# Performance work log

Measured on AMD Instinct MI355X. Metric: run time of the kernel, lower is better.

Reference implementation:

```python
import jax, jax.numpy as jnp
import numpy as np

H, HKV, D, HID = 64, 8, 64, 2880
T = 2048
WINDOW = 128
THETA = 150000.0
FACTOR = 32.0
ORIG_MAX = 4096
BETA_FAST, BETA_SLOW = 32.0, 1.0
EPS = 1e-5
SCALE = D ** -0.5
MSCALE = float(0.1 * np.log(FACTOR) + 1.0)  # vLLM YaRN attention mscale


def _yarn_inv_freq():
    # vLLM YaRNScalingRotaryEmbedding inverse frequencies
    def corr_dim(n_rot):
        return D * np.log(ORIG_MAX / (n_rot * 2.0 * np.pi)) / (2.0 * np.log(THETA))
    low = max(int(np.floor(corr_dim(BETA_FAST))), 0)
    high = min(int(np.ceil(corr_dim(BETA_SLOW))), D - 1)
    pow_ = np.arange(0, D, 2, dtype=np.float32) / D
    extrap = 1.0 / (THETA ** pow_)                 # extrapolation inv_freq
    interp = extrap / FACTOR                        # interpolation inv_freq
    ramp = np.clip((np.arange(D // 2, dtype=np.float32) - low) / max(high - low, 1e-3), 0.0, 1.0)
    extrap_mask = 1.0 - ramp
    inv_freq = interp * (1.0 - extrap_mask) + extrap * extrap_mask
    return jnp.asarray(inv_freq, jnp.float32)

_INV_FREQ = _yarn_inv_freq()


def _rope(positions, x):
    # neox-style rotation; x: [T, heads, D]
    freqs = positions.astype(jnp.float32)[:, None] * _INV_FREQ[None, :]  # [T, D/2]
    cos = (jnp.cos(freqs) * MSCALE)[:, None, :]
    sin = (jnp.sin(freqs) * MSCALE)[:, None, :]
    x1, x2 = x[..., : D // 2], x[..., D // 2 :]
    return jnp.concatenate([x1 * cos - x2 * sin, x2 * cos + x1 * sin], axis=-1)


def _attn(q, k, v, sinks):
    # q: [T,H,D]; k,v: [T,HKV,D]; sinks: [H] extra softmax logit per head
    g = H // HKV
    k = jnp.repeat(k, g, axis=1)
    v = jnp.repeat(v, g, axis=1)
    scores = jnp.einsum('qhd,khd->hqk', q, k) * SCALE  # [H,T,T]
    i = jnp.arange(T)[:, None]
    j = jnp.arange(T)[None, :]
    mask = (j <= i) & (i - j < WINDOW)  # causal + sliding window (even layer)
    scores = jnp.where(mask[None], scores, -jnp.inf)
    s = sinks[:, None]                                    # [H,1]
    m = jnp.maximum(jnp.max(scores, axis=-1), s)          # [H,T]
    p = jnp.exp(scores - m[..., None])                    # [H,T,T]
    denom = jnp.sum(p, axis=-1) + jnp.exp(s - m)          # sink adds to denominator only
    out = jnp.einsum('hqk,khd->qhd', p, v) / denom.T[..., None]
    return out.reshape(T, H * D)


def setup_inputs() -> dict:
    key = jax.random.key(0)
    ks = jax.random.split(key, 8)
    return {
        'hidden_states': jax.random.normal(ks[0], (T, HID), jnp.float32),
        'positions': jnp.arange(T, dtype=jnp.int32),
        'norm_w': jnp.ones((HID,), jnp.float32),
        'w_qkv': jax.random.normal(ks[1], ((H + 2 * HKV) * D, HID), jnp.float32) * 0.02,
        'b_qkv': jax.random.normal(ks[2], ((H + 2 * HKV) * D,), jnp.float32) * 0.02,
        'w_o': jax.random.normal(ks[3], (HID, H * D), jnp.float32) * 0.02,
        'b_o': jax.random.normal(ks[4], (HID,), jnp.float32) * 0.02,
        'sinks': jax.random.normal(ks[5], (H,), jnp.float32),
    }


def reference(hidden_states, positions, norm_w, w_qkv, b_qkv, w_o, b_o, sinks):
    x = hidden_states
    t = x * jax.lax.rsqrt(jnp.mean(x * x, axis=-1, keepdims=True) + EPS) * norm_w  # RMSNorm
    qkv = t @ w_qkv.T + b_qkv
    q, k, v = jnp.split(qkv, [H * D, H * D + HKV * D], axis=-1)
    q = _rope(positions, q.reshape(T, H, D))
    k = _rope(positions, k.reshape(T, HKV, D))
    v = v.reshape(T, HKV, D)
    attn_out = _attn(q, k, v, sinks)
    out = attn_out @ w_o.T + b_o
    return out + x  # residual
```

## Files before the change

kernel.cpp:

```cpp
#include <hip/hip_runtime.h>
#include <hip/hip_bf16.h>
#include <stdint.h>

typedef __attribute__((ext_vector_type(8))) short bf16x8;
typedef __attribute__((ext_vector_type(8))) unsigned short u16x8;
typedef __attribute__((ext_vector_type(4))) float f32x4;
typedef __attribute__((ext_vector_type(4))) unsigned short u16x4;

#define T_SEQ 2048
#define HID_D 2880
#define KPAD 2944
#define NH 64
#define NKV 8
#define HD 64
#define QKV_N 5120
#define ATT_N 4096
#define NOPAD 3072
#define WIN 128
#define RSCALE 0.125f
#define MSCALE 1.3465735903f
#define ROPE_TOT (T_SEQ * (NH + NKV) * 32)

__device__ __forceinline__ unsigned short f2bf(float f) {
  union { float f; unsigned u; } v; v.f = f;
  unsigned r = v.u + 0x7fffu + ((v.u >> 16) & 1u);
  return (unsigned short)(r >> 16);
}
__device__ __forceinline__ float bf2f(unsigned short u) {
  union { unsigned u; float f; } v; v.u = ((unsigned)u) << 16;
  return v.f;
}

__device__ __forceinline__ void gload_lds16(const void* g, void* l) {
  __builtin_amdgcn_global_load_lds((const __attribute__((address_space(1))) char*)g,
                                   (__attribute__((address_space(3))) char*)l, 16, 0, 0);
}

__global__ __launch_bounds__(256) void pre_kernel(const float* __restrict__ x,
                                                  const float* __restrict__ w,
                                                  unsigned short* __restrict__ t_bf,
                                                  const float* __restrict__ wq_src,
                                                  unsigned short* __restrict__ wq_dst) {
  __shared__ float red[256];
  if (blockIdx.x < 2048) {
    int row = blockIdx.x;
    const float4* xr4 = (const float4*)(x + (size_t)row * HID_D);
    const float4* w4 = (const float4*)w;
    float ss = 0.f;
    for (int i = threadIdx.x; i < 720; i += 256) {
      float4 v = xr4[i];
      ss += v.x * v.x + v.y * v.y + v.z * v.z + v.w * v.w;
    }
    red[threadIdx.x] = ss;
    __syncthreads();
    for (int s = 128; s > 0; s >>= 1) {
      if (threadIdx.x < s) red[threadIdx.x] += red[threadIdx.x + s];
      __syncthreads();
    }
    float rs = rsqrtf(red[0] / (float)HID_D + 1e-5f);
    u16x4* ob = (u16x4*)(t_bf + (size_t)row * KPAD);
    for (int i = threadIdx.x; i < 736; i += 256) {
      u16x4 o = {0, 0, 0, 0};
      if (i < 720) {
        float4 v = xr4[i];
        float4 g = w4[i];
        o = { f2bf(v.x * rs * g.x), f2bf(v.y * rs * g.y),
              f2bf(v.z * rs * g.z), f2bf(v.w * rs * g.w) };
      }
      ob[i] = o;
    }
  } else {
    const int total = QKV_N * 736;
    for (int i = (blockIdx.x - 2048) * 256 + threadIdx.x; i < total; i += 1024 * 256) {
      int c4 = i % 736, row = i / 736;
      u16x4 o = {0, 0, 0, 0};
      if (c4 < 720) {
        float4 v = ((const float4*)wq_src)[(size_t)row * 720 + c4];
        o = { f2bf(v.x), f2bf(v.y), f2bf(v.z), f2bf(v.w) };
      }
      ((u16x4*)wq_dst)[i] = o;
    }
  }
}

__device__ __forceinline__ void gemm_body(const unsigned short* __restrict__ A,
                                          const unsigned short* __restrict__ B,
                                          unsigned short* __restrict__ C,
                                          const float* __restrict__ bias,
                                          int N, int ld, int nt,
                                          int nbx, int nstore, int swz,
                                          unsigned short* sA, unsigned short* sB) {
  const int tid = threadIdx.x;
  const int lane = tid & 63, wid = tid >> 6;
  const int wr = wid >> 2, wc = wid & 3;
  const int lq = lane & 15, ro = lane >> 4;

  const int bx = swz % nbx, by = swz / nbx;
  const int m0 = by * 256, n0 = bx * 256;

  const int R0 = tid >> 3;
  const int g0 = (((tid & 7) ^ (R0 & 7)) << 3);
  const size_t aOff = (size_t)(m0 + R0) * ld + g0;
  size_t bOff[2][2];
#pragma unroll
  for (int h = 0; h < 2; ++h)
#pragma unroll
    for (int r = 0; r < 2; ++r) {
      int rr = n0 + h * 128 + r * 64 + R0;
      bOff[h][r] = (size_t)rr * ld + g0;
    }

  const int ck0 = ((ro ^ (lq & 7)) << 3);
  const int ck1 = (((4 + ro) ^ (lq & 7)) << 3);

#define STG_A(BUF, H, KT)                                                        \
  { unsigned short* _d = sA + ((BUF) * 2 + (H)) * 8192 + wid * 512;              \
    const unsigned short* _s = A + aOff + (size_t)((H) * 128) * ld + (KT) * 64;  \
    gload_lds16(_s, _d); gload_lds16(_s + (size_t)64 * ld, _d + 4096); }
#define STG_B(BUF, H, KT)                                                        \
  { unsigned short* _d = sB + ((BUF) * 2 + (H)) * 8192 + wid * 512;              \
    gload_lds16(B + bOff[H][0] + (KT) * 64, _d);                                 \
    gload_lds16(B + bOff[H][1] + (KT) * 64, _d + 4096); }

  bf16x8 aR[8];
  bf16x8 bR0[4], bR1[4];
  f32x4 acc[8][4] = {};

#define LDA(BUF, S)                                                                        \
  { _Pragma("unroll") for (int ii = 0; ii < 4; ++ii) {                                     \
      const int _r = ((BUF) * 2 + wr) * 8192 + ((S) * 64 + ii * 16 + lq) * 64;             \
      aR[ii * 2 + 0] = *(const bf16x8*)&sA[_r + ck0];                                      \
      aR[ii * 2 + 1] = *(const bf16x8*)&sA[_r + ck1]; } }
#define LDB(BUF, NHF, DST)                                                                 \
  { _Pragma("unroll") for (int jj = 0; jj < 2; ++jj) {                                     \
      const int _r = ((BUF) * 2 + (wc >> 1)) * 8192 +                                      \
                     ((wc & 1) * 64 + ((NHF) * 2 + jj) * 16 + lq) * 64;                    \
      DST[jj * 2 + 0] = *(const bf16x8*)&sB[_r + ck0];                                     \
      DST[jj * 2 + 1] = *(const bf16x8*)&sB[_r + ck1]; } }
#define MFMA16(S, NHF, BREG)                                                               \
  { _Pragma("unroll") for (int ii = 0; ii < 4; ++ii)                                       \
    _Pragma("unroll") for (int jj = 0; jj < 2; ++jj)                                       \
    _Pragma("unroll") for (int kk = 0; kk < 2; ++kk)                                       \
      acc[(S) * 4 + ii][(NHF) * 2 + jj] = __builtin_amdgcn_mfma_f32_16x16x32_bf16(         \
          aR[ii * 2 + kk], BREG[jj * 2 + kk], acc[(S) * 4 + ii][(NHF) * 2 + jj], 0, 0, 0); }
#define PH_MID()                                         \
  __builtin_amdgcn_s_barrier();                          \
  asm volatile("s_waitcnt lgkmcnt(0)" ::: "memory");     \
  __builtin_amdgcn_sched_barrier(0);                     \
  __builtin_amdgcn_s_setprio(1)
#define PH_END()                                         \
  __builtin_amdgcn_s_setprio(0);                         \
  __builtin_amdgcn_s_barrier()

  STG_A(0, 0, 0); STG_A(0, 1, 0); STG_B(0, 0, 0); STG_B(0, 1, 0);
  STG_B(1, 0, 1); STG_B(1, 1, 1);
  asm volatile("s_waitcnt vmcnt(4)" ::: "memory");
  __builtin_amdgcn_s_barrier();

  const int niter = nt >> 1;
  for (int it = 0; it < niter; ++it) {
    const int t = it * 2;
    const bool more = (it + 1 < niter);
    LDA(0, 0); LDB(0, 0, bR0); STG_A(1, 0, t + 1);
    PH_MID(); MFMA16(0, 0, bR0); PH_END();
    LDB(0, 1, bR1); STG_A(1, 1, t + 1);
    PH_MID(); MFMA16(0, 1, bR1); PH_END();
    LDA(0, 1); if (more) STG_B(0, 0, t + 2);
    PH_MID(); MFMA16(1, 1, bR1); PH_END();
    if (more) STG_B(0, 1, t + 2);
    PH_MID(); MFMA16(1, 0, bR0);
    __builtin_amdgcn_s_setprio(0);
    if (more) asm volatile("s_waitcnt vmcnt(4)" ::: "memory");
    else      asm volatile("s_waitcnt vmcnt(0)" ::: "memory");
    __builtin_amdgcn_s_barrier();
    LDA(1, 0); LDB(1, 0, bR0); if (more) STG_A(0, 0, t + 2);
    PH_MID(); MFMA16(0, 0, bR0); PH_END();
    LDB(1, 1, bR1); if (more) STG_A(0, 1, t + 2);
    PH_MID(); MFMA16(0, 1, bR1); PH_END();
    LDA(1, 1); if (more) STG_B(1, 0, t + 3);
    PH_MID(); MFMA16(1, 1, bR1); PH_END();
    if (more) STG_B(1, 1, t + 3);
    PH_MID(); MFMA16(1, 0, bR0);
    __builtin_amdgcn_s_setprio(0);
    if (more) asm volatile("s_waitcnt vmcnt(4)" ::: "memory");
    else      asm volatile("s_waitcnt vmcnt(0)" ::: "memory");
    __builtin_amdgcn_s_barrier();
  }
#undef STG_A
#undef STG_B
#undef LDA
#undef LDB
#undef MFMA16

#pragma unroll
  for (int fi = 0; fi < 8; ++fi) {
    const int gr = m0 + wr * 128 + fi * 16 + ro * 4;
#pragma unroll
    for (int j = 0; j < 4; ++j) {
      const int gc = n0 + wc * 64 + j * 16 + lq;
      const float bv = bias[gc];
#pragma unroll
      for (int r = 0; r < 4; ++r)
        C[(size_t)(gr + r) * nstore + gc] = f2bf(acc[fi][j][r] + bv);
    }
  }
}

__global__ __launch_bounds__(512, 2) void qkv_fused_kernel(const unsigned short* __restrict__ A,
                                                           const unsigned short* __restrict__ B,
                                                           unsigned short* __restrict__ C,
                                                           const float* __restrict__ bias,
                                                           const float* __restrict__ wo_src,
                                                           unsigned short* __restrict__ wo_dst) {
  __shared__ unsigned short sA[2 * 2 * 128 * 64];
  __shared__ unsigned short sB[2 * 2 * 128 * 64];
  const int c = blockIdx.x & 7, q = blockIdx.x >> 3;
  if (q < 20) {
    const int by = (c & 1) * 4 + (q & 3);
    const int bx = (c >> 1) * 5 + (q >> 2);
    gemm_body(A, B, C, bias, QKV_N, KPAD, 46, 20, QKV_N, by * 20 + bx, sA, sB);
  } else {
    const int cid = c * 12 + (q - 20);
    const int total = HID_D * 1024;
    for (int i = cid * 512 + threadIdx.x; i < total; i += 96 * 512) {
      float4 v = ((const float4*)wo_src)[i];
      u16x4 o = { f2bf(v.x), f2bf(v.y), f2bf(v.z), f2bf(v.w) };
      ((u16x4*)wo_dst)[i] = o;
    }
  }
}

__global__ __launch_bounds__(512, 2) void outproj192_kernel(const unsigned short* __restrict__ att,
                                                            const unsigned short* __restrict__ wo,
                                                            float* __restrict__ out,
                                                            const float* __restrict__ b_o,
                                                            const float* __restrict__ x) {
  __shared__ unsigned short sA[2 * 128 * 64];
  __shared__ unsigned short sB[3 * 192 * 64];

  const int tid = threadIdx.x;
  const int lane = tid & 63, wid = tid >> 6;
  const int wr = wid >> 2, wc = wid & 3;
  const int lq = lane & 15, ro = lane >> 4;

  const int c = blockIdx.x & 7, q = blockIdx.x >> 3;
  const int by = c * 2 + (q >= 15 ? 1 : 0);
  const int bx = (q >= 15) ? q - 15 : q;
  const int m0 = by * 128, n0 = bx * 192;

  const int R0 = tid >> 3;
  const int g0 = (((tid & 7) ^ (R0 & 7)) << 3);
  const size_t aOff = (size_t)(m0 + R0) * ATT_N + g0;
  size_t bOff[3];
#pragma unroll
  for (int r = 0; r < 3; ++r)
    bOff[r] = (size_t)(n0 + r * 64 + R0) * ATT_N + g0;

  const int ck0 = ((ro ^ (lq & 7)) << 3);
  const int ck1 = (((4 + ro) ^ (lq & 7)) << 3);

#define PSTG_A(BUF, KT)                                                         \
  { unsigned short* _d = sA + (BUF) * 8192 + wid * 512;                         \
    const unsigned short* _s = att + aOff + (size_t)(KT) * 64;                  \
    gload_lds16(_s, _d); gload_lds16(_s + (size_t)64 * ATT_N, _d + 4096); }
#define PSTG_B(BUF, KT)                                                         \
  { unsigned short* _d = sB + (BUF) * 12288 + wid * 512;                        \
    gload_lds16(wo + bOff[0] + (KT) * 64, _d);                                  \
    gload_lds16(wo + bOff[1] + (KT) * 64, _d + 4096);                           \
    gload_lds16(wo + bOff[2] + (KT) * 64, _d + 8192); }

  bf16x8 aR[8];
  bf16x8 b00, b01, b10, b11, b20, b21;
  f32x4 acc[4][3] = {};

#define PLDA(BUF)                                                                          \
  { _Pragma("unroll") for (int ii = 0; ii < 4; ++ii) {                                     \
      const int _r = (BUF) * 8192 + (wr * 64 + ii * 16 + lq) * 64;                         \
      aR[ii * 2 + 0] = *(const bf16x8*)&sA[_r + ck0];                                      \
      aR[ii * 2 + 1] = *(const bf16x8*)&sA[_r + ck1]; } }
#define PLDB(BUF, J, D0, D1)                                                               \
  { const int _r = (BUF) * 12288 + (wc * 48 + (J) * 16 + lq) * 64;                         \
    D0 = *(const bf16x8*)&sB[_r + ck0];                                                    \
    D1 = *(const bf16x8*)&sB[_r + ck1]; }

  PSTG_B(0, 0); PSTG_A(0, 0);
  PSTG_B(1, 1); PSTG_A(1, 1);
  asm volatile("s_waitcnt vmcnt(5)" ::: "memory");
  __builtin_amdgcn_s_barrier();

  const int nt = 64;
  for (int T = 0; T < nt; ++T) {
    const bool more = (T + 2 < nt);
    const int bb = T % 3, bA = T & 1;
    PLDA(bA);
    PLDB(bb, 0, b00, b01);
    PLDB(bb, 1, b10, b11);
    if (more) PSTG_B((T + 2) % 3, T + 2);
    PH_MID();
#pragma unroll
    for (int ii = 0; ii < 4; ++ii) {
      acc[ii][0] = __builtin_amdgcn_mfma_f32_16x16x32_bf16(aR[ii * 2 + 0], b00, acc[ii][0], 0, 0, 0);
      acc[ii][0] = __builtin_amdgcn_mfma_f32_16x16x32_bf16(aR[ii * 2 + 1], b01, acc[ii][0], 0, 0, 0);
      acc[ii][1] = __builtin_amdgcn_mfma_f32_16x16x32_bf16(aR[ii * 2 + 0], b10, acc[ii][1], 0, 0, 0);
      acc[ii][1] = __builtin_amdgcn_mfma_f32_16x16x32_bf16(aR[ii * 2 + 1], b11, acc[ii][1], 0, 0, 0);
    }
    PH_END();
    PLDB(bb, 2, b20, b21);
    if (more) PSTG_A((T + 2) & 1, T + 2);
    PH_MID();
#pragma unroll
    for (int ii = 0; ii < 4; ++ii) {
      acc[ii][2] = __builtin_amdgcn_mfma_f32_16x16x32_bf16(aR[ii * 2 + 0], b20, acc[ii][2], 0, 0, 0);
      acc[ii][2] = __builtin_amdgcn_mfma_f32_16x16x32_bf16(aR[ii * 2 + 1], b21, acc[ii][2], 0, 0, 0);
    }
    __builtin_amdgcn_s_setprio(0);
    if (more) asm volatile("s_waitcnt vmcnt(5)" ::: "memory");
    else      asm volatile("s_waitcnt vmcnt(0)" ::: "memory");
    __builtin_amdgcn_s_barrier();
  }
#undef PSTG_A
#undef PSTG_B
#undef PLDA
#undef PLDB
#undef PH_MID
#undef PH_END

#pragma unroll
  for (int ii = 0; ii < 4; ++ii) {
    const int gr = m0 + wr * 64 + ii * 16 + ro * 4;
#pragma unroll
    for (int j = 0; j < 3; ++j) {
      const int gc = n0 + wc * 48 + j * 16 + lq;
      const float bv = b_o[gc];
#pragma unroll
      for (int r = 0; r < 4; ++r) {
        size_t off = (size_t)(gr + r) * HID_D + gc;
        out[off] = acc[ii][j][r] + bv + x[off];
      }
    }
  }
}

__global__ __launch_bounds__(256) void ropev_kernel(const unsigned short* __restrict__ qkvb,
                                                    const int* __restrict__ positions,
                                                    unsigned short* __restrict__ qb,
                                                    unsigned short* __restrict__ kb) {
  int idx = blockIdx.x * 256 + threadIdx.x;
  int d = idx & 31;
  int head = (idx >> 5) % (NH + NKV);
  int t = idx / ((NH + NKV) * 32);
  float pw = (float)d * (1.0f / 32.0f);
  float extrap = expf(-pw * 11.9183905733f);
  float interp = extrap * (1.0f / 32.0f);
  float ramp = fminf(fmaxf(((float)d - 8.0f) * 0.1f, 0.0f), 1.0f);
  float invf = interp * ramp + extrap * (1.0f - ramp);
  float fr = (float)positions[t] * invf;
  float s, c;
  sincosf(fr, &s, &c);
  c *= MSCALE;
  s *= MSCALE;
  if (head < NH) {
    const unsigned short* b = qkvb + (size_t)t * QKV_N + head * HD + d;
    float x1 = bf2f(b[0]), x2 = bf2f(b[32]);
    unsigned short* ob = qb + (size_t)t * ATT_N + head * HD + d;
    ob[0] = f2bf(x1 * c - x2 * s);
    ob[32] = f2bf(x2 * c + x1 * s);
  } else {
    int gk = head - NH;
    const unsigned short* b = qkvb + (size_t)t * QKV_N + NH * HD + gk * HD + d;
    float x1 = bf2f(b[0]), x2 = bf2f(b[32]);
    unsigned short* ob = kb + (size_t)t * (NKV * HD) + gk * HD + d;
    ob[0] = f2bf(x1 * c - x2 * s);
    ob[32] = f2bf(x2 * c + x1 * s);
  }
}

__global__ __launch_bounds__(256) void vtrans_kernel(const unsigned short* __restrict__ qkvb,
                                                     unsigned short* __restrict__ vt) {
  __shared__ unsigned short tile[64][72];
  const int g = blockIdx.x >> 5;
  const int t0 = (blockIdx.x & 31) << 6;
  const int r = threadIdx.x >> 3;
  const int c8 = (threadIdx.x & 7) << 3;
  const size_t vbase = (size_t)(NH + NKV) * HD + (size_t)g * HD;
#pragma unroll
  for (int hh = 0; hh < 2; ++hh) {
    int row = r + hh * 32;
    *(u16x8*)&tile[row][c8] =
        *(const u16x8*)(qkvb + (size_t)(t0 + row) * QKV_N + vbase + c8);
  }
  __syncthreads();
  const int d = threadIdx.x >> 2;
  const int ts = (threadIdx.x & 3) << 4;
  u16x8 v0, v1;
#pragma unroll
  for (int i = 0; i < 8; ++i) { v0[i] = tile[ts + i][d]; v1[i] = tile[ts + 8 + i][d]; }
  unsigned short* dst = vt + (size_t)(g * HD + d) * T_SEQ + t0 + ts;
  *(u16x8*)dst = v0;
  *(u16x8*)(dst + 8) = v1;
}

__global__ __launch_bounds__(256) void attn_kernel(const unsigned short* __restrict__ qb,
                                                   const unsigned short* __restrict__ kb,
                                                   const unsigned short* __restrict__ vt,
                                                   const float* __restrict__ sinks,
                                                   unsigned short* __restrict__ att) {
  __shared__ unsigned short orep[4][16][72];
  const int lane = threadIdx.x & 63;
  const int wid = threadIdx.x >> 6;
  const int q0 = blockIdx.x * 16;
  const int h = blockIdx.y * 4 + wid;
  const int g = h >> 3;
  const int lq = lane & 15;
  const int ro = lane >> 4;

  bf16x8 bq0, bq1;
  {
    const unsigned short* qp = qb + (size_t)(q0 + lq) * ATT_N + h * HD + ro * 8;
    bq0 = *(const bf16x8*)qp;
    bq1 = *(const bf16x8*)(qp + 32);
  }
  float m_run = sinks[h];
  float l_run = 1.0f;
  f32x4 o0 = {0.f, 0.f, 0.f, 0.f}, o1 = o0, o2 = o0, o3 = o0;
  const int qg = q0 + lq;
  const int jstart = (q0 >= WIN) ? q0 - WIN : 0;

  for (int jt = jstart; jt <= q0; jt += 32) {
    f32x4 st0 = {0.f, 0.f, 0.f, 0.f}, st1 = st0;
    {
      int kr = jt + ((lq >> 2) << 3) + (lq & 3);
      int kr0 = min(kr, T_SEQ - 1);
      int kr1 = min(kr + 4, T_SEQ - 1);
      const unsigned short* kp0 = kb + (size_t)kr0 * (NKV * HD) + g * HD + ro * 8;
      const unsigned short* kp1 = kb + (size_t)kr1 * (NKV * HD) + g * HD + ro * 8;
      bf16x8 ka0a = *(const bf16x8*)kp0;
      bf16x8 ka0b = *(const bf16x8*)(kp0 + 32);
      bf16x8 ka1a = *(const bf16x8*)kp1;
      bf16x8 ka1b = *(const bf16x8*)(kp1 + 32);
      st0 = __builtin_amdgcn_mfma_f32_16x16x32_bf16(ka0a, bq0, st0, 0, 0, 0);
      st0 = __builtin_amdgcn_mfma_f32_16x16x32_bf16(ka0b, bq1, st0, 0, 0, 0);
      st1 = __builtin_amdgcn_mfma_f32_16x16x32_bf16(ka1a, bq0, st1, 0, 0, 0);
      st1 = __builtin_amdgcn_mfma_f32_16x16x32_bf16(ka1b, bq1, st1, 0, 0, 0);
    }
    float p[8];
    float tmax = -3.0e30f;
#pragma unroll
    for (int r = 0; r < 4; ++r) {
      int jg0 = jt + ro * 8 + r;
      int jg1 = jg0 + 4;
      float s0 = (jg0 <= qg && (qg - jg0) < WIN) ? st0[r] * RSCALE : -3.0e30f;
      float s1 = (jg1 <= qg && (qg - jg1) < WIN) ? st1[r] * RSCALE : -3.0e30f;
      p[r] = s0;
      p[r + 4] = s1;
      tmax = fmaxf(tmax, fmaxf(s0, s1));
    }
    tmax = fmaxf(tmax, __shfl_xor(tmax, 16));
    tmax = fmaxf(tmax, __shfl_xor(tmax, 32));
    float m_new = fmaxf(m_run, tmax);
    float rescale = expf(m_run - m_new);
    float psum = 0.f;
    bf16x8 pa;
#pragma unroll
    for (int jj = 0; jj < 8; ++jj) {
      float pe = expf(p[jj] - m_new);
      psum += pe;
      pa[jj] = (short)f2bf(pe);
    }
    psum += __shfl_xor(psum, 16);
    psum += __shfl_xor(psum, 32);
    l_run = l_run * rescale + psum;
    m_run = m_new;
    f32x4 rs4;
#pragma unroll
    for (int r = 0; r < 4; ++r) rs4[r] = __shfl(rescale, ro * 4 + r);
    o0 *= rs4; o1 *= rs4; o2 *= rs4; o3 *= rs4;
    int tb = jt + ro * 8;
    if (tb > T_SEQ - 8) tb = T_SEQ - 8;
    const unsigned short* vp = vt + (size_t)(g * HD + lq) * T_SEQ + tb;
    bf16x8 v0 = *(const bf16x8*)vp;
    bf16x8 v1 = *(const bf16x8*)(vp + 16 * T_SEQ);
    bf16x8 v2 = *(const bf16x8*)(vp + 32 * T_SEQ);
    bf16x8 v3 = *(const bf16x8*)(vp + 48 * T_SEQ);
    o0 = __builtin_amdgcn_mfma_f32_16x16x32_bf16(pa, v0, o0, 0, 0, 0);
    o1 = __builtin_amdgcn_mfma_f32_16x16x32_bf16(pa, v1, o1, 0, 0, 0);
    o2 = __builtin_amdgcn_mfma_f32_16x16x32_bf16(pa, v2, o2, 0, 0, 0);
    o3 = __builtin_amdgcn_mfma_f32_16x16x32_bf16(pa, v3, o3, 0, 0, 0);
  }

#pragma unroll
  for (int r = 0; r < 4; ++r) {
    float lr = __shfl(l_run, ro * 4 + r);
    float inv = 1.0f / lr;
    int row = ro * 4 + r;
    orep[wid][row][lq]      = f2bf(o0[r] * inv);
    orep[wid][row][lq + 16] = f2bf(o1[r] * inv);
    orep[wid][row][lq + 32] = f2bf(o2[r] * inv);
    orep[wid][row][lq + 48] = f2bf(o3[r] * inv);
  }
  {
    const int row = lane >> 2;
    const int seg = (lane & 3) << 4;
    u16x8 w0 = *(const u16x8*)&orep[wid][row][seg];
    u16x8 w1 = *(const u16x8*)&orep[wid][row][seg + 8];
    unsigned short* op = att + (size_t)(q0 + row) * ATT_N + h * HD + seg;
    *(u16x8*)op = w0;
    *(u16x8*)(op + 8) = w1;
  }
}

extern "C" void kernel_launch(void* const* d_in, const int* in_sizes, int n_in,
                              void* d_out, int out_size, void* d_ws, size_t ws_size,
                              hipStream_t stream) {
  const float* x = (const float*)d_in[0];
  const int* pos = (const int*)d_in[1];
  const float* norm_w = (const float*)d_in[2];
  const float* w_qkv = (const float*)d_in[3];
  const float* b_qkv = (const float*)d_in[4];
  const float* w_o = (const float*)d_in[5];
  const float* b_o = (const float*)d_in[6];
  const float* sinks = (const float*)d_in[7];
  float* out = (float*)d_out;

  unsigned short* t_bf = (unsigned short*)d_ws;
  unsigned short* wq_bf = t_bf + (size_t)T_SEQ * KPAD;
  unsigned short* wo_bf = wq_bf + (size_t)QKV_N * KPAD;
  unsigned short* qkv_bf = wo_bf + (size_t)NOPAD * ATT_N;
  unsigned short* qb = qkv_bf + (size_t)T_SEQ * QKV_N;
  unsigned short* kb = qb + (size_t)T_SEQ * ATT_N;
  unsigned short* vt = kb + (size_t)T_SEQ * NKV * HD;
  unsigned short* att = vt + (size_t)NKV * HD * T_SEQ;

  pre_kernel<<<3072, 256, 0, stream>>>(x, norm_w, t_bf, w_qkv, wq_bf);
  qkv_fused_kernel<<<256, 512, 0, stream>>>(t_bf, wq_bf, qkv_bf, b_qkv, w_o, wo_bf);
  ropev_kernel<<<ROPE_TOT / 256, 256, 0, stream>>>(qkv_bf, pos, qb, kb);
  vtrans_kernel<<<256, 256, 0, stream>>>(qkv_bf, vt);
  attn_kernel<<<dim3(T_SEQ / 16, NH / 4), 256, 0, stream>>>(qb, kb, vt, sinks, att);
  outproj192_kernel<<<240, 512, 0, stream>>>(att, wo_bf, out, b_o, x);
}
```

Before: 229.2 us.

## Retile QKV GEMM to 128x320 blocks and move w_o conversion into attention launch

The QKV projection GEMM moves from 160 blocks of 256x256 tiles to 256 blocks of 128x320 tiles with a triple-buffered B stage. This fills all 256 workgroup slots with GEMM work instead of reserving 96 blocks for the w_o fp32-to-bf16 conversion. That conversion is moved into 128 extra blocks prepended to the attention launch, which is flattened to a 1D grid. The intent is better CU balance for the GEMM, at the cost of lower per-block arithmetic intensity and extra work inside the attention kernel.

```diff
diff --git a/kernel.cpp b/kernel.cpp
--- a/kernel.cpp
+++ b/kernel.cpp
@@ -35,6 +35,15 @@
   __builtin_amdgcn_global_load_lds((const __attribute__((address_space(1))) char*)g,
                                    (__attribute__((address_space(3))) char*)l, 16, 0, 0);
 }
+
+#define GPH_MID()                                        \
+  __builtin_amdgcn_s_barrier();                          \
+  asm volatile("s_waitcnt lgkmcnt(0)" ::: "memory");     \
+  __builtin_amdgcn_sched_barrier(0);                     \
+  __builtin_amdgcn_s_setprio(1)
+#define GPH_END()                                        \
+  __builtin_amdgcn_s_setprio(0);                         \
+  __builtin_amdgcn_s_barrier()
 
 __global__ __launch_bounds__(256) void pre_kernel(const float* __restrict__ x,
                                                   const float* __restrict__ w,
@@ -83,149 +92,110 @@
   }
 }
 
-__device__ __forceinline__ void gemm_body(const unsigned short* __restrict__ A,
-                                          const unsigned short* __restrict__ B,
-                                          unsigned short* __restrict__ C,
-                                          const float* __restrict__ bias,
-                                          int N, int ld, int nt,
-                                          int nbx, int nstore, int swz,
-                                          unsigned short* sA, unsigned short* sB) {
+__global__ __launch_bounds__(512, 2) void qkv320_kernel(const unsigned short* __restrict__ A,
+                                                        const unsigned short* __restrict__ B,
+                                                        unsigned short* __restrict__ C,
+                                                        const float* __restrict__ bias) {
+  __shared__ unsigned short sA[2 * 128 * 64];
+  __shared__ unsigned short sB[3 * 320 * 64];
+
   const int tid = threadIdx.x;
   const int lane = tid & 63, wid = tid >> 6;
   const int wr = wid >> 2, wc = wid & 3;
   const int lq = lane & 15, ro = lane >> 4;
 
-  const int bx = swz % nbx, by = swz / nbx;
-  const int m0 = by * 256, n0 = bx * 256;
+  const int c = blockIdx.x & 7, q = blockIdx.x >> 3;
+  const int by = (c & 1) * 8 + (q & 7);
+  const int bx = (c >> 1) * 4 + (q >> 3);
+  const int m0 = by * 128, n0 = bx * 320;
 
   const int R0 = tid >> 3;
   const int g0 = (((tid & 7) ^ (R0 & 7)) << 3);
-  const size_t aOff = (size_t)(m0 + R0) * ld + g0;
-  size_t bOff[2][2];
-#pragma unroll
-  for (int h = 0; h < 2; ++h)
-#pragma unroll
-    for (int r = 0; r < 2; ++r) {
-      int rr = n0 + h * 128 + r * 64 + R0;
-      bOff[h][r] = (size_t)rr * ld + g0;
-    }
+  const size_t aOff = (size_t)(m0 + R0) * KPAD + g0;
+  size_t bOff[5];
+#pragma unroll
+  for (int r = 0; r < 5; ++r)
+    bOff[r] = (size_t)(n0 + r * 64 + R0) * KPAD + g0;
 
   const int ck0 = ((ro ^ (lq & 7)) << 3);
   const int ck1 = (((4 + ro) ^ (lq & 7)) << 3);
 
-#define STG_A(BUF, H, KT)                                                        \
-  { unsigned short* _d = sA + ((BUF) * 2 + (H)) * 8192 + wid * 512;              \
-    const unsigned short* _s = A + aOff + (size_t)((H) * 128) * ld + (KT) * 64;  \
-    gload_lds16(_s, _d); gload_lds16(_s + (size_t)64 * ld, _d + 4096); }
-#define STG_B(BUF, H, KT)                                                        \
-  { unsigned short* _d = sB + ((BUF) * 2 + (H)) * 8192 + wid * 512;              \
-    gload_lds16(B + bOff[H][0] + (KT) * 64, _d);                                 \
-    gload_lds16(B + bOff[H][1] + (KT) * 64, _d + 4096); }
+#define QSTG_A(BUF, KT)                                                         \
+  { unsigned short* _d = sA + (BUF) * 8192 + wid * 512;                         \
+    const unsigned short* _s = A + aOff + (size_t)(KT) * 64;                    \
+    gload_lds16(_s, _d); gload_lds16(_s + (size_t)64 * KPAD, _d + 4096); }
+#define QSTG_B(BUF, KT)                                                         \
+  { unsigned short* _d = sB + (BUF) * 20480 + wid * 512;                        \
+    gload_lds16(B + bOff[0] + (KT) * 64, _d);                                   \
+    gload_lds16(B + bOff[1] + (KT) * 64, _d + 4096);                            \
+    gload_lds16(B + bOff[2] + (KT) * 64, _d + 8192);                            \
+    gload_lds16(B + bOff[3] + (KT) * 64, _d + 12288);                           \
+    gload_lds16(B + bOff[4] + (KT) * 64, _d + 16384); }
 
   bf16x8 aR[8];
-  bf16x8 bR0[4], bR1[4];
-  f32x4 acc[8][4] = {};
-
-#define LDA(BUF, S)                                                                        \
+  bf16x8 b00, b01, b10, b11, b20, b21, b30, b31, b40, b41;
+  f32x4 acc[4][5] = {};
+
+#define QLDA(BUF)                                                                          \
   { _Pragma("unroll") for (int ii = 0; ii < 4; ++ii) {                                     \
-      const int _r = ((BUF) * 2 + wr) * 8192 + ((S) * 64 + ii * 16 + lq) * 64;             \
+      const int _r = (BUF) * 8192 + (wr * 64 + ii * 16 + lq) * 64;                         \
       aR[ii * 2 + 0] = *(const bf16x8*)&sA[_r + ck0];                                      \
       aR[ii * 2 + 1] = *(const bf16x8*)&sA[_r + ck1]; } }
-#define LDB(BUF, NHF, DST)                                                                 \
-  { _Pragma("unroll") for (int jj = 0; jj < 2; ++jj) {                                     \
-      const int _r = ((BUF) * 2 + (wc >> 1)) * 8192 +                                      \
-                     ((wc & 1) * 64 + ((NHF) * 2 + jj) * 16 + lq) * 64;                    \
-      DST[jj * 2 + 0] = *(const bf16x8*)&sB[_r + ck0];                                     \
-      DST[jj * 2 + 1] = *(const bf16x8*)&sB[_r + ck1]; } }
-#define MFMA16(S, NHF, BREG)                                                               \
-  { _Pragma("unroll") for (int ii = 0; ii < 4; ++ii)                                       \
-    _Pragma("unroll") for (int jj = 0; jj < 2; ++jj)                                       \
-    _Pragma("unroll") for (int kk = 0; kk < 2; ++kk)                                       \
-      acc[(S) * 4 + ii][(NHF) * 2 + jj] = __builtin_amdgcn_mfma_f32_16x16x32_bf16(         \
-          aR[ii * 2 + kk], BREG[jj * 2 + kk], acc[(S) * 4 + ii][(NHF) * 2 + jj], 0, 0, 0); }
-#define PH_MID()                                         \
-  __builtin_amdgcn_s_barrier();                          \
-  asm volatile("s_waitcnt lgkmcnt(0)" ::: "memory");     \
-  __builtin_amdgcn_sched_barrier(0);                     \
-  __builtin_amdgcn_s_setprio(1)
-#define PH_END()                                         \
-  __builtin_amdgcn_s_setprio(0);                         \
-  __builtin_amdgcn_s_barrier()
-
-  STG_A(0, 0, 0); STG_A(0, 1, 0); STG_B(0, 0, 0); STG_B(0, 1, 0);
-  STG_B(1, 0, 1); STG_B(1, 1, 1);
-  asm volatile("s_waitcnt vmcnt(4)" ::: "memory");
+#define QLDB(BUF, J, D0, D1)                                                               \
+  { const int _r = (BUF) * 20480 + (wc * 80 + (J) * 16 + lq) * 64;                         \
+    D0 = *(const bf16x8*)&sB[_r + ck0];                                                    \
+    D1 = *(const bf16x8*)&sB[_r + ck1]; }
+#define QMM(J, B0, B1)                                                                     \
+  { _Pragma("unroll") for (int ii = 0; ii < 4; ++ii) {                                     \
+      acc[ii][J] = __builtin_amdgcn_mfma_f32_16x16x32_bf16(aR[ii * 2 + 0], B0, acc[ii][J], 0, 0, 0); \
+      acc[ii][J] = __builtin_amdgcn_mfma_f32_16x16x32_bf16(aR[ii * 2 + 1], B1, acc[ii][J], 0, 0, 0); } }
+
+  QSTG_B(0, 0); QSTG_A(0, 0);
+  QSTG_B(1, 1); QSTG_A(1, 1);
+  asm volatile("s_waitcnt vmcnt(7)" ::: "memory");
   __builtin_amdgcn_s_barrier();
 
-  const int niter = nt >> 1;
-  for (int it = 0; it < niter; ++it) {
-    const int t = it * 2;
-    const bool more = (it + 1 < niter);
-    LDA(0, 0); LDB(0, 0, bR0); STG_A(1, 0, t + 1);
-    PH_MID(); MFMA16(0, 0, bR0); PH_END();
-    LDB(0, 1, bR1); STG_A(1, 1, t + 1);
-    PH_MID(); MFMA16(0, 1, bR1); PH_END();
-    LDA(0, 1); if (more) STG_B(0, 0, t + 2);
-    PH_MID(); MFMA16(1, 1, bR1); PH_END();
-    if (more) STG_B(0, 1, t + 2);
-    PH_MID(); MFMA16(1, 0, bR0);
+  const int nt = 46;
+  for (int T = 0; T < nt; ++T) {
+    const bool more = (T + 2 < nt);
+    const int bb = T % 3, bA = T & 1;
+    QLDA(bA);
+    QLDB(bb, 0, b00, b01);
+    QLDB(bb, 1, b10, b11);
+    if (more) QSTG_B((T + 2) % 3, T + 2);
+    GPH_MID();
+    QMM(0, b00, b01);
+    QMM(1, b10, b11);
+    GPH_END();
+    QLDB(bb, 2, b20, b21);
+    QLDB(bb, 3, b30, b31);
+    QLDB(bb, 4, b40, b41);
+    if (more) QSTG_A((T + 2) & 1, T + 2);
+    GPH_MID();
+    QMM(2, b20, b21);
+    QMM(3, b30, b31);
+    QMM(4, b40, b41);
     __builtin_amdgcn_s_setprio(0);
-    if (more) asm volatile("s_waitcnt vmcnt(4)" ::: "memory");
+    if (more) asm volatile("s_waitcnt vmcnt(7)" ::: "memory");
     else      asm volatile("s_waitcnt vmcnt(0)" ::: "memory");
     __builtin_amdgcn_s_barrier();
-    LDA(1, 0); LDB(1, 0, bR0); if (more) STG_A(0, 0, t + 2);
-    PH_MID(); MFMA16(0, 0, bR0); PH_END();
-    LDB(1, 1, bR1); if (more) STG_A(0, 1, t + 2);
-    PH_MID(); MFMA16(0, 1, bR1); PH_END();
-    LDA(1, 1); if (more) STG_B(1, 0, t + 3);
-    PH_MID(); MFMA16(1, 1, bR1); PH_END();
-    if (more) STG_B(1, 1, t + 3);
-    PH_MID(); MFMA16(1, 0, bR0);
-    __builtin_amdgcn_s_setprio(0);
-    if (more) asm volatile("s_waitcnt vmcnt(4)" ::: "memory");
-    else      asm volatile("s_waitcnt vmcnt(0)" ::: "memory");
-    __builtin_amdgcn_s_barrier();
-  }
-#undef STG_A
-#undef STG_B
-#undef LDA
-#undef LDB
-#undef MFMA16
-
-#pragma unroll
-  for (int fi = 0; fi < 8; ++fi) {
-    const int gr = m0 + wr * 128 + fi * 16 + ro * 4;
-#pragma unroll
-    for (int j = 0; j < 4; ++j) {
-      const int gc = n0 + wc * 64 + j * 16 + lq;
+  }
+#undef QSTG_A
+#undef QSTG_B
+#undef QLDA
+#undef QLDB
+#undef QMM
+
+#pragma unroll
+  for (int ii = 0; ii < 4; ++ii) {
+    const int gr = m0 + wr * 64 + ii * 16 + ro * 4;
+#pragma unroll
+    for (int j = 0; j < 5; ++j) {
+      const int gc = n0 + wc * 80 + j * 16 + lq;
       const float bv = bias[gc];
 #pragma unroll
       for (int r = 0; r < 4; ++r)
-        C[(size_t)(gr + r) * nstore + gc] = f2bf(acc[fi][j][r] + bv);
-    }
-  }
-}
-
-__global__ __launch_bounds__(512, 2) void qkv_fused_kernel(const unsigned short* __restrict__ A,
-                                                           const unsigned short* __restrict__ B,
-                                                           unsigned short* __restrict__ C,
-                                                           const float* __restrict__ bias,
-                                                           const float* __restrict__ wo_src,
-                                                           unsigned short* __restrict__ wo_dst) {
-  __shared__ unsigned short sA[2 * 2 * 128 * 64];
-  __shared__ unsigned short sB[2 * 2 * 128 * 64];
-  const int c = blockIdx.x & 7, q = blockIdx.x >> 3;
-  if (q < 20) {
-    const int by = (c & 1) * 4 + (q & 3);
-    const int bx = (c >> 1) * 5 + (q >> 2);
-    gemm_body(A, B, C, bias, QKV_N, KPAD, 46, 20, QKV_N, by * 20 + bx, sA, sB);
-  } else {
-    const int cid = c * 12 + (q - 20);
-    const int total = HID_D * 1024;
-    for (int i = cid * 512 + threadIdx.x; i < total; i += 96 * 512) {
-      float4 v = ((const float4*)wo_src)[i];
-      u16x4 o = { f2bf(v.x), f2bf(v.y), f2bf(v.z), f2bf(v.w) };
-      ((u16x4*)wo_dst)[i] = o;
+        C[(size_t)(gr + r) * QKV_N + gc] = f2bf(acc[ii][j][r] + bv);
     }
   }
 }
@@ -296,7 +266,7 @@
     PLDB(bb, 0, b00, b01);
     PLDB(bb, 1, b10, b11);
     if (more) PSTG_B((T + 2) % 3, T + 2);
-    PH_MID();
+    GPH_MID();
 #pragma unroll
     for (int ii = 0; ii < 4; ++ii) {
       acc[ii][0] = __builtin_amdgcn_mfma_f32_16x16x32_bf16(aR[ii * 2 + 0], b00, acc[ii][0], 0, 0, 0);
@@ -304,10 +274,10 @@
       acc[ii][1] = __builtin_amdgcn_mfma_f32_16x16x32_bf16(aR[ii * 2 + 0], b10, acc[ii][1], 0, 0, 0);
       acc[ii][1] = __builtin_amdgcn_mfma_f32_16x16x32_bf16(aR[ii * 2 + 1], b11, acc[ii][1], 0, 0, 0);
     }
-    PH_END();
+    GPH_END();
     PLDB(bb, 2, b20, b21);
     if (more) PSTG_A((T + 2) & 1, T + 2);
-    PH_MID();
+    GPH_MID();
 #pragma unroll
     for (int ii = 0; ii < 4; ++ii) {
       acc[ii][2] = __builtin_amdgcn_mfma_f32_16x16x32_bf16(aR[ii * 2 + 0], b20, acc[ii][2], 0, 0, 0);
@@ -322,8 +292,6 @@
 #undef PSTG_B
 #undef PLDA
 #undef PLDB
-#undef PH_MID
-#undef PH_END
 
 #pragma unroll
   for (int ii = 0; ii < 4; ++ii) {
@@ -404,12 +372,25 @@
                                                    const unsigned short* __restrict__ kb,
                                                    const unsigned short* __restrict__ vt,
                                                    const float* __restrict__ sinks,
-                                                   unsigned short* __restrict__ att) {
+                                                   unsigned short* __restrict__ att,
+                                                   const float* __restrict__ wo_src,
+                                                   unsigned short* __restrict__ wo_dst) {
   __shared__ unsigned short orep[4][16][72];
+  const int bid = blockIdx.x;
+  if (bid < 128) {
+    const int total = HID_D * 1024;
+    for (int i = bid * 256 + threadIdx.x; i < total; i += 128 * 256) {
+      float4 v = ((const float4*)wo_src)[i];
+      u16x4 o = { f2bf(v.x), f2bf(v.y), f2bf(v.z), f2bf(v.w) };
+      ((u16x4*)wo_dst)[i] = o;
+    }
+    return;
+  }
+  const int abid = bid - 128;
   const int lane = threadIdx.x & 63;
   const int wid = threadIdx.x >> 6;
-  const int q0 = blockIdx.x * 16;
-  const int h = blockIdx.y * 4 + wid;
+  const int q0 = (abid & 127) * 16;
+  const int h = (abid >> 7) * 4 + wid;
   const int g = h >> 3;
   const int lq = lane & 15;
   const int ro = lane >> 4;
@@ -532,9 +513,9 @@
   unsigned short* att = vt + (size_t)NKV * HD * T_SEQ;
 
   pre_kernel<<<3072, 256, 0, stream>>>(x, norm_w, t_bf, w_qkv, wq_bf);
-  qkv_fused_kernel<<<256, 512, 0, stream>>>(t_bf, wq_bf, qkv_bf, b_qkv, w_o, wo_bf);
+  qkv320_kernel<<<256, 512, 0, stream>>>(t_bf, wq_bf, qkv_bf, b_qkv);
   ropev_kernel<<<ROPE_TOT / 256, 256, 0, stream>>>(qkv_bf, pos, qb, kb);
   vtrans_kernel<<<256, 256, 0, stream>>>(qkv_bf, vt);
-  attn_kernel<<<dim3(T_SEQ / 16, NH / 4), 256, 0, stream>>>(qb, kb, vt, sinks, att);
+  attn_kernel<<<2176, 256, 0, stream>>>(qb, kb, vt, sinks, att, w_o, wo_bf);
   outproj192_kernel<<<240, 512, 0, stream>>>(att, wo_bf, out, b_o, x);
 }
```

Measured after the change: 244.5 us. +6.7%, slower.
